# Optimization experiments

Hardware: AMD Instinct MI355X
Metric: run time of the kernel (lower is better)

Reference implementation:

```python
import jax, jax.numpy as jnp
import numpy as np
import math

B, S, E, H, L = 32, 512, 256, 8, 2
Dh = E // H
NUM_Q, NUM_C, MAX_POS, R = 10000, 200, 512, 4


def setup_inputs() -> dict:
    key = jax.random.key(0)
    ks = jax.random.split(key, 32)
    f = lambda k, sh: (jax.random.normal(k, sh, jnp.float32) * 0.05)
    que_emb = f(ks[0], (NUM_Q + 1, E)).at[0].set(0.0)  # padding_idx=0
    inp = dict(
        pid_data=jax.random.randint(ks[1], (B, S), 0, NUM_Q + 1),
        c_data=jax.random.randint(ks[2], (B, S, R), 0, NUM_C),
        target=jax.random.randint(ks[3], (B, S), 0, 2),
        que_emb=que_emb,
        concept_emb=f(ks[4], (NUM_C, E)),
        pos_key_emb=f(ks[5], (MAX_POS, Dh)),
        pos_value_emb=f(ks[6], (MAX_POS, Dh)),
        qc_W=f(ks[7], (2 * E, E)), qc_b=jnp.zeros((E,), jnp.float32),
        lin_W=f(ks[8], (2 * E, E)), lin_b=jnp.zeros((E,), jnp.float32),
        Wq=f(ks[9], (L, E, E)), bq=jnp.zeros((L, E), jnp.float32),
        Wk=f(ks[10], (L, E, E)), bk=jnp.zeros((L, E), jnp.float32),
        Wv=f(ks[11], (L, E, E)), bv=jnp.zeros((L, E), jnp.float32),
        o1_W=f(ks[12], (2 * E, E)), o1_b=jnp.zeros((E,), jnp.float32),
        o2_W=f(ks[13], (E, E)), o2_b=jnp.zeros((E,), jnp.float32),
        o3_W=f(ks[14], (E, 1)), o3_b=jnp.zeros((1,), jnp.float32),
    )
    return inp


def _relative_attention(q_in, v_in, Wq, bq, Wk, bk, Wv, bv, pos_key_emb, pos_value_emb):
    b, s, e = q_in.shape
    proj = lambda x, W, bias: (x @ W + bias).reshape(b, s, H, Dh).transpose(0, 2, 1, 3)
    q = proj(q_in, Wq, bq)  # [b,h,s,dh]
    k = proj(q_in, Wk, bk)
    v = proj(v_in, Wv, bv)
    # relative position indices, clamped (Shaw et al. variant)
    i = jnp.arange(s)
    idxs = jnp.clip(i[:, None] - i[None, :], 0, MAX_POS - 1)  # [s,s]
    pos_k = pos_key_emb[idxs]    # [s,s,dh]
    pos_v = pos_value_emb[idxs]  # [s,s,dh]
    scores = jnp.einsum('bhid,bhjd->bhij', q, k) + jnp.einsum('bhid,ijd->bhij', q, pos_k)
    scores = scores / math.sqrt(Dh)
    # future_mask: triu with k=0 -> mask j >= i (incl. diagonal)
    causal = (i[None, :] >= i[:, None])  # [s,s] True where masked
    scores = jnp.where(causal, jnp.float32(-1e9), scores)
    p = jax.nn.softmax(scores, axis=-1)  # [b,h,i,j]
    # pad-zero trick: row i=0 of attention replaced by zeros
    p = p * (i[:, None] > 0).astype(p.dtype)
    # value = v + per-pair positional value bias
    out = jnp.einsum('bhij,bhjd->bhid', p, v) + jnp.einsum('bhij,ijd->bhid', p, pos_v)
    return out.transpose(0, 2, 1, 3).reshape(b, s, E), p


def reference(pid_data, c_data, target, que_emb, concept_emb, pos_key_emb,
              pos_value_emb, qc_W, qc_b, lin_W, lin_b, Wq, bq, Wk, bk, Wv, bv,
              o1_W, o1_b, o2_W, o2_b, o3_W, o3_b):
    qemb = que_emb[pid_data]  # [B,S,E]
    # average skill embedding; index 0 of padded table is the zero/pad row
    concept_cat = jnp.concatenate([jnp.zeros((1, E), concept_emb.dtype), concept_emb], axis=0)
    related = c_data + 1  # [B,S,R]
    cemb_sum = concept_cat[related].sum(axis=-2)  # [B,S,E]
    cnt = (related != 0).sum(axis=-1, keepdims=True)
    cnt = jnp.maximum(cnt, 1)
    cemb = cemb_sum / cnt.astype(cemb_sum.dtype)
    query = jnp.concatenate([qemb, cemb], axis=-1) @ qc_W + qc_b  # [B,S,E]
    # interaction embedding gated by response label
    lbl = target[..., None].astype(query.dtype)
    inter = jnp.concatenate([query * lbl, query * (1.0 - lbl)], axis=-1)
    inter = jax.nn.relu(inter @ lin_W + lin_b)  # [B,S,E]
    sim = jax.nn.sigmoid(jnp.einsum('bse,ce->bsc', qemb, concept_emb))
    outputs, _ = _relative_attention(query, inter, Wq[0], bq[0], Wk[0], bk[0],
                                     Wv[0], bv[0], pos_key_emb, pos_value_emb)
    for l in range(1, L):
        residual, _ = _relative_attention(outputs, inter, Wq[l], bq[l], Wk[l], bk[l],
                                          Wv[l], bv[l], pos_key_emb, pos_value_emb)
        outputs = outputs + jax.nn.relu(residual)
    h = jnp.concatenate([outputs, query], axis=-1)
    h = jax.nn.relu(h @ o1_W + o1_b)
    h = jax.nn.relu(h @ o2_W + o2_b)
    pred = jax.nn.sigmoid((h @ o3_W + o3_b).squeeze(-1))  # [B,S]
    return pred, sim
```

## Files before the change

### kernel.cpp

```cpp
#include <hip/hip_runtime.h>
#include <hip/hip_bf16.h>
#include <cmath>

#define B_   32
#define S_   512
#define E_   256
#define H_   8
#define DH_  32
#define L_   2
#define R_   4
#define NUMC_ 200
#define MAXPOS_ 512
#define MTOK (B_ * S_)

typedef __attribute__((ext_vector_type(8))) short bf16x8_t;
typedef __attribute__((ext_vector_type(4))) float f32x4_t;

__device__ inline ushort bfu(float a) {
    union { __hip_bfloat16 h; ushort u; } x; x.h = __float2bfloat16(a); return x.u;
}
__device__ inline uint pk2bf(float a, float b) {
    return (uint)bfu(a) | ((uint)bfu(b) << 16);
}
__device__ inline float bf2f(ushort u) {
    union { float f; uint u; } x; x.u = (uint)u << 16; return x.f;
}
__device__ inline __hip_bfloat16 f2bf(float a) { return __float2bfloat16(a); }

__global__ __launch_bounds__(256) void wcvt_k(
    const float* __restrict__ qcW, const float* __restrict__ linW,
    const float* __restrict__ Wq, const float* __restrict__ Wk,
    const float* __restrict__ Wv, const float* __restrict__ o1W,
    const float* __restrict__ o2W, const float* __restrict__ ce,
    const float* __restrict__ posk, const float* __restrict__ posv,
    __hip_bfloat16* __restrict__ wb,
    __hip_bfloat16* __restrict__ pkPad, __hip_bfloat16* __restrict__ pvT)
{
    if (blockIdx.x >= 3584) {
        int t = (blockIdx.x - 3584) * 256 + threadIdx.x;
        {
            int row = t >> 5, d = t & 31;
            int rel = row - 32;
            float v = (rel >= 0 && rel < MAXPOS_) ? posk[(size_t)rel * DH_ + d] : 0.f;
            pkPad[t] = f2bf(v);
        }
        {
            int d = t / 576, c = t - d * 576;
            int rel = c - 31;
            float v = (rel >= 0 && rel < MAXPOS_) ? posv[(size_t)rel * DH_ + d] : 0.f;
            pvT[t] = f2bf(v);
        }
        return;
    }
    int i = blockIdx.x * 256 + threadIdx.x;
    float v;
    if (i < 131072) {
        int n = i >> 9, k = i & 511; v = qcW[k * 256 + n];
    } else if (i < 262144) {
        int l = i - 131072; int n = l >> 9, k = l & 511; v = linW[k * 256 + n];
    } else if (i < 524288) {
        int l2 = i - 262144; int ly = l2 >> 17; int r2 = l2 & 131071;
        int n = r2 >> 8, k = r2 & 255;
        v = (n < 256) ? Wq[ly * 65536 + k * 256 + n]
                      : Wk[ly * 65536 + k * 256 + (n - 256)];
    } else if (i < 655360) {
        int l2 = i - 524288; int n = l2 >> 8, k = l2 & 255;
        int ly = n >> 8, nn = n & 255;
        v = Wv[ly * 65536 + k * 256 + nn];
    } else if (i < 786432) {
        int l = i - 655360; int n = l >> 9, k = l & 511; v = o1W[k * 256 + n];
    } else if (i < 851968) {
        int l = i - 786432; int n = l >> 8, k = l & 255; v = o2W[k * 256 + n];
    } else {
        int l = i - 851968; int c = l >> 8, k = l & 255;
        v = (c < NUMC_) ? ce[c * 256 + k] : 0.f;
    }
    wb[i] = f2bf(v);
}

__global__ __launch_bounds__(256) void embed_k(
    const int* __restrict__ pid, const int* __restrict__ cdat,
    const float* __restrict__ qe, const float* __restrict__ ce,
    __hip_bfloat16* __restrict__ qemb, __hip_bfloat16* __restrict__ cemb)
{
    int tkn = blockIdx.x * 4 + (threadIdx.x >> 6);
    int e4  = (threadIdx.x & 63) * 4;
    int p = pid[tkn];
    float4 q = *reinterpret_cast<const float4*>(qe + (size_t)p * E_ + e4);
    ushort4 qo; qo.x = bfu(q.x); qo.y = bfu(q.y); qo.z = bfu(q.z); qo.w = bfu(q.w);
    *reinterpret_cast<ushort4*>(qemb + (size_t)tkn * E_ + e4) = qo;
    const int* c = cdat + (size_t)tkn * R_;
    float4 s = make_float4(0.f, 0.f, 0.f, 0.f);
#pragma unroll
    for (int r = 0; r < R_; ++r) {
        float4 v = *reinterpret_cast<const float4*>(ce + (size_t)c[r] * E_ + e4);
        s.x += v.x; s.y += v.y; s.z += v.z; s.w += v.w;
    }
    ushort4 co; co.x = bfu(s.x * 0.25f); co.y = bfu(s.y * 0.25f);
    co.z = bfu(s.z * 0.25f); co.w = bfu(s.w * 0.25f);
    *reinterpret_cast<ushort4*>(cemb + (size_t)tkn * E_ + e4) = co;
}

template<int AMODE, int EPI, int OMODE, int K, int NB>
__global__ __launch_bounds__(256) void gemm_bf_k(
    const __hip_bfloat16* __restrict__ A0, const __hip_bfloat16* __restrict__ A1,
    const int* __restrict__ lbl,
    const __hip_bfloat16* __restrict__ BT,
    const float* __restrict__ bias, const float* __restrict__ bias2,
    void* __restrict__ C0, void* __restrict__ C1, int Nstride)
{
    const int lane = threadIdx.x & 63, w = threadIdx.x >> 6;
    const int col = lane & 15, rg = lane >> 4;
    const int wr = w >> 1, wc = w & 1;
    int did = blockIdx.y * gridDim.x + blockIdx.x;
    int bm, bn;
    if (NB == 512) {
        int swz = (did & 7) * 128 + (did >> 3);
        bm = (swz >> 2) * 64; bn = (swz & 3) * 128;
    } else {
        int swz = (did & 7) * 64 + (did >> 3);
        bm = (swz >> 1) * 64; bn = (swz & 1) * 128;
    }
    const f32x4_t z4 = {0.f, 0.f, 0.f, 0.f};
    f32x4_t acc[2][4] = {{z4, z4, z4, z4}, {z4, z4, z4, z4}};
    const bf16x8_t z8 = {0, 0, 0, 0, 0, 0, 0, 0};

    int rowA[2];
    rowA[0] = bm + wr * 32 + col;
    rowA[1] = bm + wr * 32 + 16 + col;
    int lblv[2] = {0, 0};
    if (AMODE == 2) { lblv[0] = lbl[rowA[0]]; lblv[1] = lbl[rowA[1]]; }
    const int nb0 = bn + wc * 64;

    for (int k0 = 0; k0 < K; k0 += 32) {
        const int kk = k0 + 8 * rg;
        bf16x8_t af[2], bfr[4];
#pragma unroll
        for (int mt = 0; mt < 2; ++mt) {
            if (AMODE == 0) {
                af[mt] = *reinterpret_cast<const bf16x8_t*>(A0 + (size_t)rowA[mt] * K + kk);
            } else if (AMODE == 1) {
                const __hip_bfloat16* p = (kk < 256) ? (A0 + (size_t)rowA[mt] * 256 + kk)
                                                     : (A1 + (size_t)rowA[mt] * 256 + (kk - 256));
                af[mt] = *reinterpret_cast<const bf16x8_t*>(p);
            } else {
                bf16x8_t a = *reinterpret_cast<const bf16x8_t*>(A0 + (size_t)rowA[mt] * 256 + (kk & 255));
                bool first = (kk < 256);
                af[mt] = ((lblv[mt] != 0) == first) ? a : z8;
            }
        }
#pragma unroll
        for (int nt = 0; nt < 4; ++nt)
            bfr[nt] = *reinterpret_cast<const bf16x8_t*>(BT + (size_t)(nb0 + nt * 16 + col) * K + kk);

        __builtin_amdgcn_s_setprio(1);
#pragma unroll
        for (int mt = 0; mt < 2; ++mt)
#pragma unroll
        for (int nt = 0; nt < 4; ++nt)
            acc[mt][nt] = __builtin_amdgcn_mfma_f32_16x16x32_bf16(af[mt], bfr[nt], acc[mt][nt], 0, 0, 0);
        __builtin_amdgcn_s_setprio(0);
    }

#pragma unroll
    for (int mt = 0; mt < 2; ++mt)
#pragma unroll
    for (int nt = 0; nt < 4; ++nt) {
        const int n = nb0 + nt * 16 + col;
        const int mb = bm + wr * 32 + mt * 16 + 4 * rg;
        float bs = 0.f;
        if (bias) bs = (NB == 512 && n >= 256) ? bias2[n - 256] : bias[n];
        float xv[4];
#pragma unroll
        for (int r = 0; r < 4; ++r) {
            float x = acc[mt][nt][r] + bs;
            if (EPI == 1) x = fmaxf(x, 0.f);
            else if (EPI == 2) x = 1.f / (1.f + expf(-x));
            xv[r] = x;
        }
        if (OMODE == 0) {
            if (n < Nstride) {
                float* C = (float*)C0;
#pragma unroll
                for (int r = 0; r < 4; ++r)
                    C[(size_t)(mb + r) * Nstride + n] = xv[r];
            }
        } else if (OMODE == 3) {
            __hip_bfloat16* Cb = (__hip_bfloat16*)C0;
#pragma unroll
            for (int r = 0; r < 4; ++r)
                Cb[(size_t)(mb + r) * 256 + n] = f2bf(xv[r]);
        } else if (OMODE == 1) {
            __hip_bfloat16* dst = (n < 256) ? (__hip_bfloat16*)C0 : (__hip_bfloat16*)C1;
            const int nn = n & 255, hh = nn >> 5, d = nn & 31;
#pragma unroll
            for (int r = 0; r < 4; ++r) {
                int m = mb + r;
                int bh = (m >> 9) * 8 + hh;
                dst[((size_t)bh * 512 + (m & 511)) * 32 + d] = f2bf(xv[r]);
            }
        } else {
            __hip_bfloat16* dst = (n < 256) ? (__hip_bfloat16*)C0 : (__hip_bfloat16*)C1;
            const int nn = n & 255, hh = nn >> 5, d = nn & 31;
            const int bh = (mb >> 9) * 8 + hh;
            ushort4 pk;
            pk.x = bfu(xv[0]); pk.y = bfu(xv[1]); pk.z = bfu(xv[2]); pk.w = bfu(xv[3]);
            *reinterpret_cast<ushort4*>(dst + ((size_t)bh * 32 + d) * 512 + (mb & 511)) = pk;
        }
    }
}

__global__ __launch_bounds__(256) void gemm_pred_k(
    const __hip_bfloat16* __restrict__ A0, const __hip_bfloat16* __restrict__ BT,
    const float* __restrict__ b2, const float* __restrict__ w3,
    const float* __restrict__ b3, float* __restrict__ pred)
{
    __shared__ float sl[2][64];
    const int lane = threadIdx.x & 63, w = threadIdx.x >> 6;
    const int col = lane & 15, rg = lane >> 4;
    const int wr = w >> 1, wc = w & 1;
    const int bm = blockIdx.x * 64;

    const f32x4_t z4 = {0.f, 0.f, 0.f, 0.f};
    f32x4_t acc[2][8];
#pragma unroll
    for (int mt = 0; mt < 2; ++mt)
#pragma unroll
    for (int nt = 0; nt < 8; ++nt) acc[mt][nt] = z4;

    int rowA[2];
    rowA[0] = bm + wr * 32 + col;
    rowA[1] = bm + wr * 32 + 16 + col;
    const int nb0 = wc * 128;

    for (int k0 = 0; k0 < 256; k0 += 32) {
        const int kk = k0 + 8 * rg;
        bf16x8_t af[2], bfr[8];
#pragma unroll
        for (int mt = 0; mt < 2; ++mt)
            af[mt] = *reinterpret_cast<const bf16x8_t*>(A0 + (size_t)rowA[mt] * 256 + kk);
#pragma unroll
        for (int nt = 0; nt < 8; ++nt)
            bfr[nt] = *reinterpret_cast<const bf16x8_t*>(BT + (size_t)(nb0 + nt * 16 + col) * 256 + kk);
        __builtin_amdgcn_s_setprio(1);
#pragma unroll
        for (int mt = 0; mt < 2; ++mt)
#pragma unroll
        for (int nt = 0; nt < 8; ++nt)
            acc[mt][nt] = __builtin_amdgcn_mfma_f32_16x16x32_bf16(af[mt], bfr[nt], acc[mt][nt], 0, 0, 0);
        __builtin_amdgcn_s_setprio(0);
    }

    float pr[2][4] = {};
#pragma unroll
    for (int mt = 0; mt < 2; ++mt)
#pragma unroll
    for (int nt = 0; nt < 8; ++nt) {
        const int n = nb0 + nt * 16 + col;
        float bs = b2[n], wv = w3[n];
#pragma unroll
        for (int r = 0; r < 4; ++r)
            pr[mt][r] += fmaxf(acc[mt][nt][r] + bs, 0.f) * wv;
    }
#pragma unroll
    for (int mt = 0; mt < 2; ++mt)
#pragma unroll
    for (int r = 0; r < 4; ++r) {
        float v = pr[mt][r];
        v += __shfl_xor(v, 1); v += __shfl_xor(v, 2);
        v += __shfl_xor(v, 4); v += __shfl_xor(v, 8);
        if (col == 0) sl[wc][wr * 32 + mt * 16 + 4 * rg + r] = v;
    }
    __syncthreads();
    if (threadIdx.x < 64) {
        float s = sl[0][threadIdx.x] + sl[1][threadIdx.x] + b3[0];
        pred[bm + threadIdx.x] = 1.f / (1.f + expf(-s));
    }
}

#define QPST 36
template<int ADDREL>
__global__ __launch_bounds__(64) void attn1w_k(
    const __hip_bfloat16* __restrict__ Qbf, const __hip_bfloat16* __restrict__ Kbf,
    const __hip_bfloat16* __restrict__ Vt,  const __hip_bfloat16* __restrict__ pkPad,
    const __hip_bfloat16* __restrict__ pvT, __hip_bfloat16* __restrict__ outp)
{
    __shared__ __align__(16) ushort ldsA[64 * QPST];
    __shared__ __align__(16) ushort ldsP[2304];

    const int lane = threadIdx.x;
    const int col = lane & 15, rg = lane >> 4;
    const int bh = blockIdx.x, b = bh >> 3, h = bh & 7;
    const int band = 15 - blockIdx.y;
    const int i0 = band * 32;
    const int nT = band + 1;

    {
        uint4 zz = make_uint4(0u, 0u, 0u, 0u);
        uint4* pz = reinterpret_cast<uint4*>(ldsP);
#pragma unroll
        for (int t = 0; t < 5; ++t) {
            int idx = lane + 64 * t;
            if (idx < 288) pz[idx] = zz;
        }
    }

    const __hip_bfloat16* Qb = Qbf + (size_t)bh * 512 * 32;
    const __hip_bfloat16* Kb = Kbf + (size_t)bh * 512 * 32;
    const __hip_bfloat16* Vb = Vt  + (size_t)bh * 32 * 512;

    bf16x8_t qf[2];
    qf[0] = *reinterpret_cast<const bf16x8_t*>(Qb + (size_t)(i0 + col) * 32 + 8 * rg);
    qf[1] = *reinterpret_cast<const bf16x8_t*>(Qb + (size_t)(i0 + 16 + col) * 32 + 8 * rg);

    const f32x4_t z4 = {0.f, 0.f, 0.f, 0.f};
    f32x4_t o[2][2] = {{z4, z4}, {z4, z4}};
    float lrow[2][4] = {};
    const float rscale = 0.17677669529663687f;

    for (int t = 0; t < nT; ++t) {
        const int j0 = t * 32;
        bf16x8_t kf0 = *reinterpret_cast<const bf16x8_t*>(Kb + (size_t)(j0 + col) * 32 + 8 * rg);
        bf16x8_t kf1 = *reinterpret_cast<const bf16x8_t*>(Kb + (size_t)(j0 + 16 + col) * 32 + 8 * rg);
        const int prow0 = i0 - j0 + 1;
        bf16x8_t pkf[4];
#pragma unroll
        for (int rt = 0; rt < 4; ++rt)
            pkf[rt] = *reinterpret_cast<const bf16x8_t*>(
                pkPad + (size_t)(prow0 + rt * 16 + col) * 32 + 8 * rg);

        __builtin_amdgcn_s_setprio(1);
        f32x4_t sA[2][2];
        sA[0][0] = __builtin_amdgcn_mfma_f32_16x16x32_bf16(qf[0], kf0, z4, 0, 0, 0);
        sA[0][1] = __builtin_amdgcn_mfma_f32_16x16x32_bf16(qf[0], kf1, z4, 0, 0, 0);
        sA[1][0] = __builtin_amdgcn_mfma_f32_16x16x32_bf16(qf[1], kf0, z4, 0, 0, 0);
        sA[1][1] = __builtin_amdgcn_mfma_f32_16x16x32_bf16(qf[1], kf1, z4, 0, 0, 0);
        f32x4_t qp0[4], qp1[4];
#pragma unroll
        for (int rt = 0; rt < 4; ++rt) {
            qp0[rt] = __builtin_amdgcn_mfma_f32_16x16x32_bf16(qf[0], pkf[rt], z4, 0, 0, 0);
            qp1[rt] = __builtin_amdgcn_mfma_f32_16x16x32_bf16(qf[1], pkf[rt], z4, 0, 0, 0);
        }
        __builtin_amdgcn_s_setprio(0);

#pragma unroll
        for (int rt = 0; rt < 4; ++rt) {
            int xo = (rt * 16 + col) * QPST;
            uint2 wv;
            wv.x = pk2bf(qp0[rt][0], qp0[rt][1]);
            wv.y = pk2bf(qp0[rt][2], qp0[rt][3]);
            *reinterpret_cast<uint2*>(&ldsA[xo + 4 * rg]) = wv;
            wv.x = pk2bf(qp1[rt][0], qp1[rt][1]);
            wv.y = pk2bf(qp1[rt][2], qp1[rt][3]);
            *reinterpret_cast<uint2*>(&ldsA[xo + 16 + 4 * rg]) = wv;
        }

        const bool diag = (j0 == i0);
        float ev[2][2][4];
#pragma unroll
        for (int mt = 0; mt < 2; ++mt)
#pragma unroll
        for (int r = 0; r < 4; ++r) {
            const int ii = mt * 16 + 4 * rg + r;
#pragma unroll
            for (int nt = 0; nt < 2; ++nt) {
                const int jj = nt * 16 + col;
                float qpv = bf2f(ldsA[(ii - jj + 31) * QPST + ii]);
                float sc = (sA[mt][nt][r] + qpv) * rscale;
                float e = __expf(sc);
                if (diag && jj >= ii) e = 0.f;
                ev[mt][nt][r] = e;
            }
            lrow[mt][r] += ev[mt][0][r] + ev[mt][1][r];
        }

#pragma unroll
        for (int mt = 0; mt < 2; ++mt)
#pragma unroll
        for (int nt = 0; nt < 2; ++nt)
#pragma unroll
        for (int r = 0; r < 4; ++r) {
            const int ii = mt * 16 + 4 * rg + r;
            const int jj = nt * 16 + col;
            ushort pe = bfu(ev[mt][nt][r]);
            ldsA[ii * 32 + (jj ^ ((ii & 3) << 3))] = pe;
            ldsP[ii * 72 + (ii - jj + 31)] = pe;
        }

        bf16x8_t pa0 = *reinterpret_cast<const bf16x8_t*>(&ldsA[col * 32 + (8 * rg ^ ((col & 3) << 3))]);
        bf16x8_t pa1 = *reinterpret_cast<const bf16x8_t*>(&ldsA[(16 + col) * 32 + (8 * rg ^ ((col & 3) << 3))]);
        bf16x8_t vf0 = *reinterpret_cast<const bf16x8_t*>(Vb + (size_t)col * 512 + j0 + 8 * rg);
        bf16x8_t vf1 = *reinterpret_cast<const bf16x8_t*>(Vb + (size_t)(16 + col) * 512 + j0 + 8 * rg);
        bf16x8_t pr0[2], pr1[2], pv0[2], pv1[2];
#pragma unroll
        for (int ks = 0; ks < 2; ++ks) {
            pr0[ks] = *reinterpret_cast<const bf16x8_t*>(&ldsP[col * 72 + ks * 32 + 8 * rg]);
            pr1[ks] = *reinterpret_cast<const bf16x8_t*>(&ldsP[(16 + col) * 72 + ks * 32 + 8 * rg]);
            const __hip_bfloat16* pvb = pvT + (i0 - j0) + ks * 32 + 8 * rg;
            pv0[ks] = *reinterpret_cast<const bf16x8_t*>(pvb + (size_t)col * 576);
            pv1[ks] = *reinterpret_cast<const bf16x8_t*>(pvb + (size_t)(16 + col) * 576);
        }
        __builtin_amdgcn_s_setprio(1);
        o[0][0] = __builtin_amdgcn_mfma_f32_16x16x32_bf16(pa0, vf0, o[0][0], 0, 0, 0);
        o[0][1] = __builtin_amdgcn_mfma_f32_16x16x32_bf16(pa0, vf1, o[0][1], 0, 0, 0);
        o[1][0] = __builtin_amdgcn_mfma_f32_16x16x32_bf16(pa1, vf0, o[1][0], 0, 0, 0);
        o[1][1] = __builtin_amdgcn_mfma_f32_16x16x32_bf16(pa1, vf1, o[1][1], 0, 0, 0);
#pragma unroll
        for (int ks = 0; ks < 2; ++ks) {
            o[0][0] = __builtin_amdgcn_mfma_f32_16x16x32_bf16(pr0[ks], pv0[ks], o[0][0], 0, 0, 0);
            o[0][1] = __builtin_amdgcn_mfma_f32_16x16x32_bf16(pr0[ks], pv1[ks], o[0][1], 0, 0, 0);
            o[1][0] = __builtin_amdgcn_mfma_f32_16x16x32_bf16(pr1[ks], pv0[ks], o[1][0], 0, 0, 0);
            o[1][1] = __builtin_amdgcn_mfma_f32_16x16x32_bf16(pr1[ks], pv1[ks], o[1][1], 0, 0, 0);
        }
        __builtin_amdgcn_s_setprio(0);
    }

#pragma unroll
    for (int mt = 0; mt < 2; ++mt)
#pragma unroll
    for (int r = 0; r < 4; ++r) {
        float ls = lrow[mt][r];
        ls += __shfl_xor(ls, 1); ls += __shfl_xor(ls, 2);
        ls += __shfl_xor(ls, 4); ls += __shfl_xor(ls, 8);
        const int i = i0 + mt * 16 + 4 * rg + r;
        float inv = (i == 0) ? 0.f : 1.0f / ls;
        __hip_bfloat16* orow = outp + (size_t)(b * 512 + i) * 256 + h * 32;
        float v0 = o[mt][0][r] * inv;
        float v1 = o[mt][1][r] * inv;
        if (ADDREL) {
            v0 = bf2f(*(ushort*)&orow[col])      + fmaxf(v0, 0.f);
            v1 = bf2f(*(ushort*)&orow[16 + col]) + fmaxf(v1, 0.f);
        }
        orow[col]      = f2bf(v0);
        orow[16 + col] = f2bf(v1);
    }
}

extern "C" void kernel_launch(void* const* d_in, const int* in_sizes, int n_in,
                              void* d_out, int out_size, void* d_ws, size_t ws_size,
                              hipStream_t stream)
{
    const int*   pid        = (const int*)d_in[0];
    const int*   cdat       = (const int*)d_in[1];
    const int*   target     = (const int*)d_in[2];
    const float* que_emb    = (const float*)d_in[3];
    const float* concept_emb= (const float*)d_in[4];
    const float* posk       = (const float*)d_in[5];
    const float* posv       = (const float*)d_in[6];
    const float* qcW        = (const float*)d_in[7];
    const float* qcb        = (const float*)d_in[8];
    const float* linW       = (const float*)d_in[9];
    const float* linb       = (const float*)d_in[10];
    const float* Wq         = (const float*)d_in[11];
    const float* bq         = (const float*)d_in[12];
    const float* Wk         = (const float*)d_in[13];
    const float* bk         = (const float*)d_in[14];
    const float* Wv         = (const float*)d_in[15];
    const float* bv         = (const float*)d_in[16];
    const float* o1W        = (const float*)d_in[17];
    const float* o1b        = (const float*)d_in[18];
    const float* o2W        = (const float*)d_in[19];
    const float* o2b        = (const float*)d_in[20];
    const float* o3W        = (const float*)d_in[21];
    const float* o3b        = (const float*)d_in[22];

    float* out  = (float*)d_out;
    float* pred = out;
    float* sim  = out + MTOK;

    __hip_bfloat16* wsb = (__hip_bfloat16*)d_ws;
    const size_t HB = (size_t)MTOK * E_;
    __hip_bfloat16* qemb  = wsb + 0 * HB;
    __hip_bfloat16* cemb  = wsb + 1 * HB;
    __hip_bfloat16* query = wsb + 2 * HB;
    __hip_bfloat16* inter = wsb + 3 * HB;
    __hip_bfloat16* qbuf  = wsb + 4 * HB;
    __hip_bfloat16* kbuf  = wsb + 5 * HB;
    __hip_bfloat16* v0    = wsb + 6 * HB;
    __hip_bfloat16* v1    = wsb + 7 * HB;
    __hip_bfloat16* outp  = wsb + 8 * HB;
    __hip_bfloat16* h1    = wsb + 9 * HB;
    __hip_bfloat16* wb    = wsb + 10 * HB;
    __hip_bfloat16* qcWT  = wb;
    __hip_bfloat16* linWT = wb + 131072;
    __hip_bfloat16* wqkT  = wb + 262144;
    __hip_bfloat16* wvT   = wb + 524288;
    __hip_bfloat16* o1WT  = wb + 655360;
    __hip_bfloat16* o2WT  = wb + 786432;
    __hip_bfloat16* ceT   = wb + 851968;
    __hip_bfloat16* pkPad = wb + 917504;
    __hip_bfloat16* pvT   = pkPad + 18432;

    dim3 blk(256);
    dim3 g256(2, 256);
    dim3 g512(4, 256);
    dim3 gattn(B_ * H_, 16);
    dim3 blk64(64);

    wcvt_k<<<3656, blk, 0, stream>>>(qcW, linW, Wq, Wk, Wv, o1W, o2W, concept_emb,
                                     posk, posv, wb, pkPad, pvT);
    embed_k<<<MTOK / 4, blk, 0, stream>>>(pid, cdat, que_emb, concept_emb, qemb, cemb);

    gemm_bf_k<1, 0, 3, 512, 256><<<g256, blk, 0, stream>>>(qemb, cemb, nullptr, qcWT, qcb, nullptr, query, nullptr, 256);
    gemm_bf_k<2, 1, 3, 512, 256><<<g256, blk, 0, stream>>>(query, nullptr, target, linWT, linb, nullptr, inter, nullptr, 256);
    gemm_bf_k<0, 2, 0, 256, 256><<<g256, blk, 0, stream>>>(qemb, nullptr, nullptr, ceT, nullptr, nullptr, sim, nullptr, 200);
    gemm_bf_k<0, 0, 2, 256, 512><<<g512, blk, 0, stream>>>(inter, nullptr, nullptr, wvT, bv, bv + 256, v0, v1, 0);

    gemm_bf_k<0, 0, 1, 256, 512><<<g512, blk, 0, stream>>>(query, nullptr, nullptr, wqkT, bq, bk, qbuf, kbuf, 0);
    attn1w_k<0><<<gattn, blk64, 0, stream>>>(qbuf, kbuf, v0, pkPad, pvT, outp);

    gemm_bf_k<0, 0, 1, 256, 512><<<g512, blk, 0, stream>>>(outp, nullptr, nullptr, wqkT + 131072, bq + 256, bk + 256, qbuf, kbuf, 0);
    attn1w_k<1><<<gattn, blk64, 0, stream>>>(qbuf, kbuf, v1, pkPad, pvT, outp);

    gemm_bf_k<1, 1, 3, 512, 256><<<g256, blk, 0, stream>>>(outp, query, nullptr, o1WT, o1b, nullptr, h1, nullptr, 256);
    gemm_pred_k<<<256, blk, 0, stream>>>(h1, o2WT, o2b, o3W, o3b, pred);
}
```

Measured before the change: 290.7 us.

## Split attention query bands from 32 to 16 rows per wave

The single-wave attention kernel now handles 16 query rows per block instead of 32, doubling the grid in the band dimension. Per-block register and LDS footprint shrink (one Q fragment, three positional-key tiles, smaller scratch), and the causal mask moves to the last key tile. The aim is more parallelism and occupancy, with a shorter critical path for the longest bands. The cost is that K, V and positional tiles are loaded twice as often overall, and diagonal tiles do some masked work.

```diff
diff --git a/kernel.cpp b/kernel.cpp
--- a/kernel.cpp
+++ b/kernel.cpp
@@ -278,30 +278,30 @@
     }
 }
 
-#define QPST 36
+#define QPST 20
 template<int ADDREL>
 __global__ __launch_bounds__(64) void attn1w_k(
     const __hip_bfloat16* __restrict__ Qbf, const __hip_bfloat16* __restrict__ Kbf,
     const __hip_bfloat16* __restrict__ Vt,  const __hip_bfloat16* __restrict__ pkPad,
     const __hip_bfloat16* __restrict__ pvT, __hip_bfloat16* __restrict__ outp)
 {
-    __shared__ __align__(16) ushort ldsA[64 * QPST];
-    __shared__ __align__(16) ushort ldsP[2304];
+    __shared__ __align__(16) ushort ldsA[48 * QPST];
+    __shared__ __align__(16) ushort ldsP[16 * 72];
 
     const int lane = threadIdx.x;
     const int col = lane & 15, rg = lane >> 4;
     const int bh = blockIdx.x, b = bh >> 3, h = bh & 7;
-    const int band = 15 - blockIdx.y;
-    const int i0 = band * 32;
-    const int nT = band + 1;
+    const int band = 31 - (int)blockIdx.y;
+    const int i0 = band * 16;
+    const int nT = (band >> 1) + 1;
 
     {
         uint4 zz = make_uint4(0u, 0u, 0u, 0u);
         uint4* pz = reinterpret_cast<uint4*>(ldsP);
 #pragma unroll
-        for (int t = 0; t < 5; ++t) {
+        for (int t = 0; t < 3; ++t) {
             int idx = lane + 64 * t;
-            if (idx < 288) pz[idx] = zz;
+            if (idx < 144) pz[idx] = zz;
         }
     }
 
@@ -309,13 +309,11 @@
     const __hip_bfloat16* Kb = Kbf + (size_t)bh * 512 * 32;
     const __hip_bfloat16* Vb = Vt  + (size_t)bh * 32 * 512;
 
-    bf16x8_t qf[2];
-    qf[0] = *reinterpret_cast<const bf16x8_t*>(Qb + (size_t)(i0 + col) * 32 + 8 * rg);
-    qf[1] = *reinterpret_cast<const bf16x8_t*>(Qb + (size_t)(i0 + 16 + col) * 32 + 8 * rg);
+    bf16x8_t qf = *reinterpret_cast<const bf16x8_t*>(Qb + (size_t)(i0 + col) * 32 + 8 * rg);
 
     const f32x4_t z4 = {0.f, 0.f, 0.f, 0.f};
-    f32x4_t o[2][2] = {{z4, z4}, {z4, z4}};
-    float lrow[2][4] = {};
+    f32x4_t o[2] = {z4, z4};
+    float lrow[4] = {};
     const float rscale = 0.17677669529663687f;
 
     for (int t = 0; t < nT; ++t) {
@@ -323,110 +321,91 @@
         bf16x8_t kf0 = *reinterpret_cast<const bf16x8_t*>(Kb + (size_t)(j0 + col) * 32 + 8 * rg);
         bf16x8_t kf1 = *reinterpret_cast<const bf16x8_t*>(Kb + (size_t)(j0 + 16 + col) * 32 + 8 * rg);
         const int prow0 = i0 - j0 + 1;
-        bf16x8_t pkf[4];
-#pragma unroll
-        for (int rt = 0; rt < 4; ++rt)
+        bf16x8_t pkf[3];
+#pragma unroll
+        for (int rt = 0; rt < 3; ++rt)
             pkf[rt] = *reinterpret_cast<const bf16x8_t*>(
                 pkPad + (size_t)(prow0 + rt * 16 + col) * 32 + 8 * rg);
 
         __builtin_amdgcn_s_setprio(1);
-        f32x4_t sA[2][2];
-        sA[0][0] = __builtin_amdgcn_mfma_f32_16x16x32_bf16(qf[0], kf0, z4, 0, 0, 0);
-        sA[0][1] = __builtin_amdgcn_mfma_f32_16x16x32_bf16(qf[0], kf1, z4, 0, 0, 0);
-        sA[1][0] = __builtin_amdgcn_mfma_f32_16x16x32_bf16(qf[1], kf0, z4, 0, 0, 0);
-        sA[1][1] = __builtin_amdgcn_mfma_f32_16x16x32_bf16(qf[1], kf1, z4, 0, 0, 0);
-        f32x4_t qp0[4], qp1[4];
-#pragma unroll
-        for (int rt = 0; rt < 4; ++rt) {
-            qp0[rt] = __builtin_amdgcn_mfma_f32_16x16x32_bf16(qf[0], pkf[rt], z4, 0, 0, 0);
-            qp1[rt] = __builtin_amdgcn_mfma_f32_16x16x32_bf16(qf[1], pkf[rt], z4, 0, 0, 0);
-        }
+        f32x4_t sA[2];
+        sA[0] = __builtin_amdgcn_mfma_f32_16x16x32_bf16(qf, kf0, z4, 0, 0, 0);
+        sA[1] = __builtin_amdgcn_mfma_f32_16x16x32_bf16(qf, kf1, z4, 0, 0, 0);
+        f32x4_t qp[3];
+#pragma unroll
+        for (int rt = 0; rt < 3; ++rt)
+            qp[rt] = __builtin_amdgcn_mfma_f32_16x16x32_bf16(qf, pkf[rt], z4, 0, 0, 0);
         __builtin_amdgcn_s_setprio(0);
 
 #pragma unroll
-        for (int rt = 0; rt < 4; ++rt) {
+        for (int rt = 0; rt < 3; ++rt) {
             int xo = (rt * 16 + col) * QPST;
             uint2 wv;
-            wv.x = pk2bf(qp0[rt][0], qp0[rt][1]);
-            wv.y = pk2bf(qp0[rt][2], qp0[rt][3]);
+            wv.x = pk2bf(qp[rt][0], qp[rt][1]);
+            wv.y = pk2bf(qp[rt][2], qp[rt][3]);
             *reinterpret_cast<uint2*>(&ldsA[xo + 4 * rg]) = wv;
-            wv.x = pk2bf(qp1[rt][0], qp1[rt][1]);
-            wv.y = pk2bf(qp1[rt][2], qp1[rt][3]);
-            *reinterpret_cast<uint2*>(&ldsA[xo + 16 + 4 * rg]) = wv;
-        }
-
-        const bool diag = (j0 == i0);
-        float ev[2][2][4];
-#pragma unroll
-        for (int mt = 0; mt < 2; ++mt)
+        }
+
+        const bool last = (t == nT - 1);
+        float ev[2][4];
 #pragma unroll
         for (int r = 0; r < 4; ++r) {
-            const int ii = mt * 16 + 4 * rg + r;
+            const int ii = 4 * rg + r;
 #pragma unroll
             for (int nt = 0; nt < 2; ++nt) {
                 const int jj = nt * 16 + col;
                 float qpv = bf2f(ldsA[(ii - jj + 31) * QPST + ii]);
-                float sc = (sA[mt][nt][r] + qpv) * rscale;
+                float sc = (sA[nt][r] + qpv) * rscale;
                 float e = __expf(sc);
-                if (diag && jj >= ii) e = 0.f;
-                ev[mt][nt][r] = e;
+                if (last && (j0 + jj >= i0 + ii)) e = 0.f;
+                ev[nt][r] = e;
             }
-            lrow[mt][r] += ev[mt][0][r] + ev[mt][1][r];
-        }
-
-#pragma unroll
-        for (int mt = 0; mt < 2; ++mt)
+            lrow[r] += ev[0][r] + ev[1][r];
+        }
+
 #pragma unroll
         for (int nt = 0; nt < 2; ++nt)
 #pragma unroll
         for (int r = 0; r < 4; ++r) {
-            const int ii = mt * 16 + 4 * rg + r;
+            const int ii = 4 * rg + r;
             const int jj = nt * 16 + col;
-            ushort pe = bfu(ev[mt][nt][r]);
+            ushort pe = bfu(ev[nt][r]);
             ldsA[ii * 32 + (jj ^ ((ii & 3) << 3))] = pe;
             ldsP[ii * 72 + (ii - jj + 31)] = pe;
         }
 
-        bf16x8_t pa0 = *reinterpret_cast<const bf16x8_t*>(&ldsA[col * 32 + (8 * rg ^ ((col & 3) << 3))]);
-        bf16x8_t pa1 = *reinterpret_cast<const bf16x8_t*>(&ldsA[(16 + col) * 32 + (8 * rg ^ ((col & 3) << 3))]);
+        bf16x8_t pa = *reinterpret_cast<const bf16x8_t*>(&ldsA[col * 32 + (8 * rg ^ ((col & 3) << 3))]);
         bf16x8_t vf0 = *reinterpret_cast<const bf16x8_t*>(Vb + (size_t)col * 512 + j0 + 8 * rg);
         bf16x8_t vf1 = *reinterpret_cast<const bf16x8_t*>(Vb + (size_t)(16 + col) * 512 + j0 + 8 * rg);
-        bf16x8_t pr0[2], pr1[2], pv0[2], pv1[2];
+        bf16x8_t pr[2], pv0[2], pv1[2];
 #pragma unroll
         for (int ks = 0; ks < 2; ++ks) {
-            pr0[ks] = *reinterpret_cast<const bf16x8_t*>(&ldsP[col * 72 + ks * 32 + 8 * rg]);
-            pr1[ks] = *reinterpret_cast<const bf16x8_t*>(&ldsP[(16 + col) * 72 + ks * 32 + 8 * rg]);
+            pr[ks] = *reinterpret_cast<const bf16x8_t*>(&ldsP[col * 72 + ks * 32 + 8 * rg]);
             const __hip_bfloat16* pvb = pvT + (i0 - j0) + ks * 32 + 8 * rg;
             pv0[ks] = *reinterpret_cast<const bf16x8_t*>(pvb + (size_t)col * 576);
             pv1[ks] = *reinterpret_cast<const bf16x8_t*>(pvb + (size_t)(16 + col) * 576);
         }
         __builtin_amdgcn_s_setprio(1);
-        o[0][0] = __builtin_amdgcn_mfma_f32_16x16x32_bf16(pa0, vf0, o[0][0], 0, 0, 0);
-        o[0][1] = __builtin_amdgcn_mfma_f32_16x16x32_bf16(pa0, vf1, o[0][1], 0, 0, 0);
-        o[1][0] = __builtin_amdgcn_mfma_f32_16x16x32_bf16(pa1, vf0, o[1][0], 0, 0, 0);
-        o[1][1] = __builtin_amdgcn_mfma_f32_16x16x32_bf16(pa1, vf1, o[1][1], 0, 0, 0);
+        o[0] = __builtin_amdgcn_mfma_f32_16x16x32_bf16(pa, vf0, o[0], 0, 0, 0);
+        o[1] = __builtin_amdgcn_mfma_f32_16x16x32_bf16(pa, vf1, o[1], 0, 0, 0);
 #pragma unroll
         for (int ks = 0; ks < 2; ++ks) {
-            o[0][0] = __builtin_amdgcn_mfma_f32_16x16x32_bf16(pr0[ks], pv0[ks], o[0][0], 0, 0, 0);
-            o[0][1] = __builtin_amdgcn_mfma_f32_16x16x32_bf16(pr0[ks], pv1[ks], o[0][1], 0, 0, 0);
-            o[1][0] = __builtin_amdgcn_mfma_f32_16x16x32_bf16(pr1[ks], pv0[ks], o[1][0], 0, 0, 0);
-            o[1][1] = __builtin_amdgcn_mfma_f32_16x16x32_bf16(pr1[ks], pv1[ks], o[1][1], 0, 0, 0);
+            o[0] = __builtin_amdgcn_mfma_f32_16x16x32_bf16(pr[ks], pv0[ks], o[0], 0, 0, 0);
+            o[1] = __builtin_amdgcn_mfma_f32_16x16x32_bf16(pr[ks], pv1[ks], o[1], 0, 0, 0);
         }
         __builtin_amdgcn_s_setprio(0);
     }
 
 #pragma unroll
-    for (int mt = 0; mt < 2; ++mt)
-#pragma unroll
     for (int r = 0; r < 4; ++r) {
-        float ls = lrow[mt][r];
+        float ls = lrow[r];
         ls += __shfl_xor(ls, 1); ls += __shfl_xor(ls, 2);
         ls += __shfl_xor(ls, 4); ls += __shfl_xor(ls, 8);
-        const int i = i0 + mt * 16 + 4 * rg + r;
+        const int i = i0 + 4 * rg + r;
         float inv = (i == 0) ? 0.f : 1.0f / ls;
         __hip_bfloat16* orow = outp + (size_t)(b * 512 + i) * 256 + h * 32;
-        float v0 = o[mt][0][r] * inv;
-        float v1 = o[mt][1][r] * inv;
+        float v0 = o[0][r] * inv;
+        float v1 = o[1][r] * inv;
         if (ADDREL) {
             v0 = bf2f(*(ushort*)&orow[col])      + fmaxf(v0, 0.f);
             v1 = bf2f(*(ushort*)&orow[16 + col]) + fmaxf(v1, 0.f);
@@ -494,7 +473,7 @@
     dim3 blk(256);
     dim3 g256(2, 256);
     dim3 g512(4, 256);
-    dim3 gattn(B_ * H_, 16);
+    dim3 gattn(B_ * H_, 32);
     dim3 blk64(64);
 
     wcvt_k<<<3656, blk, 0, stream>>>(qcW, linW, Wq, Wk, Wv, o1W, o2W, concept_emb,
```

New measurement: 350.0 us. +20.4%, slower.

## Fuse sim GEMM into query projection and fuse head MLP GEMMs

Applied to the files above, without the earlier changes.

Concatenates the padded concept embedding into the query-projection weight so one GEMM produces both query and sigmoid similarity. Fuses the o1 and o2 GEMMs and prediction head into one kernel keeping the hidden activations in LDS, removing the h1 buffer round-trip and two launches. Also vectorizes the weight conversion kernel to 8 elements per thread. The merged GEMM does redundant MFMA work on zero-padded K for the sim columns.

```diff
diff --git a/kernel.cpp b/kernel.cpp
--- a/kernel.cpp
+++ b/kernel.cpp
@@ -36,8 +36,8 @@
     __hip_bfloat16* __restrict__ wb,
     __hip_bfloat16* __restrict__ pkPad, __hip_bfloat16* __restrict__ pvT)
 {
-    if (blockIdx.x >= 3584) {
-        int t = (blockIdx.x - 3584) * 256 + threadIdx.x;
+    if (blockIdx.x >= 480) {
+        int t = (blockIdx.x - 480) * 256 + threadIdx.x;
         {
             int row = t >> 5, d = t & 31;
             int rel = row - 32;
@@ -52,30 +52,53 @@
         }
         return;
     }
-    int i = blockIdx.x * 256 + threadIdx.x;
-    float v;
-    if (i < 131072) {
-        int n = i >> 9, k = i & 511; v = qcW[k * 256 + n];
-    } else if (i < 262144) {
-        int l = i - 131072; int n = l >> 9, k = l & 511; v = linW[k * 256 + n];
-    } else if (i < 524288) {
-        int l2 = i - 262144; int ly = l2 >> 17; int r2 = l2 & 131071;
-        int n = r2 >> 8, k = r2 & 255;
-        v = (n < 256) ? Wq[ly * 65536 + k * 256 + n]
-                      : Wk[ly * 65536 + k * 256 + (n - 256)];
-    } else if (i < 655360) {
-        int l2 = i - 524288; int n = l2 >> 8, k = l2 & 255;
-        int ly = n >> 8, nn = n & 255;
-        v = Wv[ly * 65536 + k * 256 + nn];
-    } else if (i < 786432) {
-        int l = i - 655360; int n = l >> 9, k = l & 511; v = o1W[k * 256 + n];
-    } else if (i < 851968) {
-        int l = i - 786432; int n = l >> 8, k = l & 255; v = o2W[k * 256 + n];
+    int id8 = blockIdx.x * 256 + threadIdx.x;
+    float v[8];
+    size_t dst;
+    if (id8 < 16384) {
+        int n = id8 & 255, k0 = (id8 >> 8) * 8;
+#pragma unroll
+        for (int j = 0; j < 8; ++j) v[j] = qcW[(size_t)(k0 + j) * 256 + n];
+        dst = (size_t)n * 512 + k0;
+    } else if (id8 < 32768) {
+        int l = id8 - 16384; int c = l & 255, k0 = (l >> 8) * 8;
+#pragma unroll
+        for (int j = 0; j < 8; ++j)
+            v[j] = (c < NUMC_ && k0 < 256) ? ce[(size_t)c * 256 + k0 + j] : 0.f;
+        dst = 131072 + (size_t)c * 512 + k0;
+    } else if (id8 < 49152) {
+        int l = id8 - 32768; int n = l & 255, k0 = (l >> 8) * 8;
+#pragma unroll
+        for (int j = 0; j < 8; ++j) v[j] = linW[(size_t)(k0 + j) * 256 + n];
+        dst = 262144 + (size_t)n * 512 + k0;
+    } else if (id8 < 81920) {
+        int l = id8 - 49152; int n2 = l & 1023, k0 = (l >> 10) * 8;
+        int ly = n2 >> 9, n = n2 & 511;
+        const float* src = (n < 256) ? (Wq + ly * 65536 + n) : (Wk + ly * 65536 + (n - 256));
+#pragma unroll
+        for (int j = 0; j < 8; ++j) v[j] = src[(size_t)(k0 + j) * 256];
+        dst = 393216 + (size_t)n2 * 256 + k0;
+    } else if (id8 < 98304) {
+        int l = id8 - 81920; int n = l & 511, k0 = (l >> 9) * 8;
+        const float* src = Wv + (n >> 8) * 65536 + (n & 255);
+#pragma unroll
+        for (int j = 0; j < 8; ++j) v[j] = src[(size_t)(k0 + j) * 256];
+        dst = 655360 + (size_t)n * 256 + k0;
+    } else if (id8 < 114688) {
+        int l = id8 - 98304; int n = l & 255, k0 = (l >> 8) * 8;
+#pragma unroll
+        for (int j = 0; j < 8; ++j) v[j] = o1W[(size_t)(k0 + j) * 256 + n];
+        dst = 786432 + (size_t)n * 512 + k0;
     } else {
-        int l = i - 851968; int c = l >> 8, k = l & 255;
-        v = (c < NUMC_) ? ce[c * 256 + k] : 0.f;
-    }
-    wb[i] = f2bf(v);
+        int l = id8 - 114688; int n = l & 255, k0 = (l >> 8) * 8;
+#pragma unroll
+        for (int j = 0; j < 8; ++j) v[j] = o2W[(size_t)(k0 + j) * 256 + n];
+        dst = 917504 + (size_t)n * 256 + k0;
+    }
+    union { ushort u[8]; uint4 q; } pk;
+#pragma unroll
+    for (int j = 0; j < 8; ++j) pk.u[j] = bfu(v[j]);
+    *reinterpret_cast<uint4*>(wb + dst) = pk.q;
 }
 
 __global__ __launch_bounds__(256) void embed_k(
@@ -169,13 +192,15 @@
         const int n = nb0 + nt * 16 + col;
         const int mb = bm + wr * 32 + mt * 16 + 4 * rg;
         float bs = 0.f;
-        if (bias) bs = (NB == 512 && n >= 256) ? bias2[n - 256] : bias[n];
+        if (OMODE == 4) bs = (n < 256 && bias) ? bias[n] : 0.f;
+        else if (bias) bs = (NB == 512 && n >= 256) ? bias2[n - 256] : bias[n];
         float xv[4];
 #pragma unroll
         for (int r = 0; r < 4; ++r) {
             float x = acc[mt][nt][r] + bs;
             if (EPI == 1) x = fmaxf(x, 0.f);
             else if (EPI == 2) x = 1.f / (1.f + expf(-x));
+            if (OMODE == 4 && n >= 256) x = 1.f / (1.f + expf(-x));
             xv[r] = x;
         }
         if (OMODE == 0) {
@@ -190,6 +215,18 @@
 #pragma unroll
             for (int r = 0; r < 4; ++r)
                 Cb[(size_t)(mb + r) * 256 + n] = f2bf(xv[r]);
+        } else if (OMODE == 4) {
+            if (n < 256) {
+                __hip_bfloat16* Cb = (__hip_bfloat16*)C0;
+#pragma unroll
+                for (int r = 0; r < 4; ++r)
+                    Cb[(size_t)(mb + r) * 256 + n] = f2bf(xv[r]);
+            } else if (n - 256 < NUMC_) {
+                float* S = (float*)C1;
+#pragma unroll
+                for (int r = 0; r < 4; ++r)
+                    S[(size_t)(mb + r) * NUMC_ + (n - 256)] = xv[r];
+            }
         } else if (OMODE == 1) {
             __hip_bfloat16* dst = (n < 256) ? (__hip_bfloat16*)C0 : (__hip_bfloat16*)C1;
             const int nn = n & 255, hh = nn >> 5, d = nn & 31;
@@ -210,66 +247,114 @@
     }
 }
 
-__global__ __launch_bounds__(256) void gemm_pred_k(
-    const __hip_bfloat16* __restrict__ A0, const __hip_bfloat16* __restrict__ BT,
-    const float* __restrict__ b2, const float* __restrict__ w3,
-    const float* __restrict__ b3, float* __restrict__ pred)
+#define HST 264
+__global__ __launch_bounds__(256) void head_k(
+    const __hip_bfloat16* __restrict__ A0, const __hip_bfloat16* __restrict__ A1,
+    const __hip_bfloat16* __restrict__ o1WT, const float* __restrict__ b1,
+    const __hip_bfloat16* __restrict__ o2WT, const float* __restrict__ b2,
+    const float* __restrict__ w3, const float* __restrict__ b3,
+    float* __restrict__ pred)
 {
+    __shared__ __align__(16) ushort ldsH[64 * HST];
     __shared__ float sl[2][64];
     const int lane = threadIdx.x & 63, w = threadIdx.x >> 6;
     const int col = lane & 15, rg = lane >> 4;
     const int wr = w >> 1, wc = w & 1;
     const int bm = blockIdx.x * 64;
-
+    const int nb0 = wc * 128;
     const f32x4_t z4 = {0.f, 0.f, 0.f, 0.f};
-    f32x4_t acc[2][8];
-#pragma unroll
-    for (int mt = 0; mt < 2; ++mt)
-#pragma unroll
-    for (int nt = 0; nt < 8; ++nt) acc[mt][nt] = z4;
 
     int rowA[2];
     rowA[0] = bm + wr * 32 + col;
     rowA[1] = bm + wr * 32 + 16 + col;
-    const int nb0 = wc * 128;
-
-    for (int k0 = 0; k0 < 256; k0 += 32) {
-        const int kk = k0 + 8 * rg;
-        bf16x8_t af[2], bfr[8];
-#pragma unroll
-        for (int mt = 0; mt < 2; ++mt)
-            af[mt] = *reinterpret_cast<const bf16x8_t*>(A0 + (size_t)rowA[mt] * 256 + kk);
-#pragma unroll
-        for (int nt = 0; nt < 8; ++nt)
-            bfr[nt] = *reinterpret_cast<const bf16x8_t*>(BT + (size_t)(nb0 + nt * 16 + col) * 256 + kk);
-        __builtin_amdgcn_s_setprio(1);
-#pragma unroll
-        for (int mt = 0; mt < 2; ++mt)
-#pragma unroll
-        for (int nt = 0; nt < 8; ++nt)
-            acc[mt][nt] = __builtin_amdgcn_mfma_f32_16x16x32_bf16(af[mt], bfr[nt], acc[mt][nt], 0, 0, 0);
-        __builtin_amdgcn_s_setprio(0);
-    }
-
-    float pr[2][4] = {};
-#pragma unroll
-    for (int mt = 0; mt < 2; ++mt)
-#pragma unroll
-    for (int nt = 0; nt < 8; ++nt) {
-        const int n = nb0 + nt * 16 + col;
-        float bs = b2[n], wv = w3[n];
-#pragma unroll
-        for (int r = 0; r < 4; ++r)
-            pr[mt][r] += fmaxf(acc[mt][nt][r] + bs, 0.f) * wv;
-    }
-#pragma unroll
-    for (int mt = 0; mt < 2; ++mt)
-#pragma unroll
-    for (int r = 0; r < 4; ++r) {
-        float v = pr[mt][r];
-        v += __shfl_xor(v, 1); v += __shfl_xor(v, 2);
-        v += __shfl_xor(v, 4); v += __shfl_xor(v, 8);
-        if (col == 0) sl[wc][wr * 32 + mt * 16 + 4 * rg + r] = v;
+
+    {
+        f32x4_t acc[2][8];
+#pragma unroll
+        for (int mt = 0; mt < 2; ++mt)
+#pragma unroll
+        for (int nt = 0; nt < 8; ++nt) acc[mt][nt] = z4;
+
+        for (int k0 = 0; k0 < 512; k0 += 32) {
+            const int kk = k0 + 8 * rg;
+            bf16x8_t af[2], bfr[8];
+#pragma unroll
+            for (int mt = 0; mt < 2; ++mt) {
+                const __hip_bfloat16* p = (kk < 256) ? (A0 + (size_t)rowA[mt] * 256 + kk)
+                                                     : (A1 + (size_t)rowA[mt] * 256 + (kk - 256));
+                af[mt] = *reinterpret_cast<const bf16x8_t*>(p);
+            }
+#pragma unroll
+            for (int nt = 0; nt < 8; ++nt)
+                bfr[nt] = *reinterpret_cast<const bf16x8_t*>(o1WT + (size_t)(nb0 + nt * 16 + col) * 512 + kk);
+            __builtin_amdgcn_s_setprio(1);
+#pragma unroll
+            for (int mt = 0; mt < 2; ++mt)
+#pragma unroll
+            for (int nt = 0; nt < 8; ++nt)
+                acc[mt][nt] = __builtin_amdgcn_mfma_f32_16x16x32_bf16(af[mt], bfr[nt], acc[mt][nt], 0, 0, 0);
+            __builtin_amdgcn_s_setprio(0);
+        }
+#pragma unroll
+        for (int mt = 0; mt < 2; ++mt)
+#pragma unroll
+        for (int nt = 0; nt < 8; ++nt) {
+            const int n = nb0 + nt * 16 + col;
+            const float bs = b1[n];
+            const int rb = wr * 32 + mt * 16 + 4 * rg;
+#pragma unroll
+            for (int r = 0; r < 4; ++r)
+                ldsH[(rb + r) * HST + n] = bfu(fmaxf(acc[mt][nt][r] + bs, 0.f));
+        }
+    }
+    __syncthreads();
+
+    {
+        f32x4_t acc[2][8];
+#pragma unroll
+        for (int mt = 0; mt < 2; ++mt)
+#pragma unroll
+        for (int nt = 0; nt < 8; ++nt) acc[mt][nt] = z4;
+
+        for (int k0 = 0; k0 < 256; k0 += 32) {
+            const int kk = k0 + 8 * rg;
+            bf16x8_t af[2], bfr[8];
+#pragma unroll
+            for (int mt = 0; mt < 2; ++mt)
+                af[mt] = *reinterpret_cast<const bf16x8_t*>(
+                    &ldsH[(wr * 32 + mt * 16 + col) * HST + kk]);
+#pragma unroll
+            for (int nt = 0; nt < 8; ++nt)
+                bfr[nt] = *reinterpret_cast<const bf16x8_t*>(o2WT + (size_t)(nb0 + nt * 16 + col) * 256 + kk);
+            __builtin_amdgcn_s_setprio(1);
+#pragma unroll
+            for (int mt = 0; mt < 2; ++mt)
+#pragma unroll
+            for (int nt = 0; nt < 8; ++nt)
+                acc[mt][nt] = __builtin_amdgcn_mfma_f32_16x16x32_bf16(af[mt], bfr[nt], acc[mt][nt], 0, 0, 0);
+            __builtin_amdgcn_s_setprio(0);
+        }
+
+        float pr[2][4] = {};
+#pragma unroll
+        for (int mt = 0; mt < 2; ++mt)
+#pragma unroll
+        for (int nt = 0; nt < 8; ++nt) {
+            const int n = nb0 + nt * 16 + col;
+            float bs = b2[n], wv = w3[n];
+#pragma unroll
+            for (int r = 0; r < 4; ++r)
+                pr[mt][r] += fmaxf(acc[mt][nt][r] + bs, 0.f) * wv;
+        }
+#pragma unroll
+        for (int mt = 0; mt < 2; ++mt)
+#pragma unroll
+        for (int r = 0; r < 4; ++r) {
+            float v = pr[mt][r];
+            v += __shfl_xor(v, 1); v += __shfl_xor(v, 2);
+            v += __shfl_xor(v, 4); v += __shfl_xor(v, 8);
+            if (col == 0) sl[wc][wr * 32 + mt * 16 + 4 * rg + r] = v;
+        }
     }
     __syncthreads();
     if (threadIdx.x < 64) {
@@ -479,16 +564,14 @@
     __hip_bfloat16* v0    = wsb + 6 * HB;
     __hip_bfloat16* v1    = wsb + 7 * HB;
     __hip_bfloat16* outp  = wsb + 8 * HB;
-    __hip_bfloat16* h1    = wsb + 9 * HB;
-    __hip_bfloat16* wb    = wsb + 10 * HB;
-    __hip_bfloat16* qcWT  = wb;
-    __hip_bfloat16* linWT = wb + 131072;
-    __hip_bfloat16* wqkT  = wb + 262144;
-    __hip_bfloat16* wvT   = wb + 524288;
-    __hip_bfloat16* o1WT  = wb + 655360;
-    __hip_bfloat16* o2WT  = wb + 786432;
-    __hip_bfloat16* ceT   = wb + 851968;
-    __hip_bfloat16* pkPad = wb + 917504;
+    __hip_bfloat16* wb    = wsb + 9 * HB;
+    __hip_bfloat16* qcCe  = wb;
+    __hip_bfloat16* linWT = wb + 262144;
+    __hip_bfloat16* wqkT  = wb + 393216;
+    __hip_bfloat16* wvT   = wb + 655360;
+    __hip_bfloat16* o1WT  = wb + 786432;
+    __hip_bfloat16* o2WT  = wb + 917504;
+    __hip_bfloat16* pkPad = wb + 983040;
     __hip_bfloat16* pvT   = pkPad + 18432;
 
     dim3 blk(256);
@@ -497,13 +580,12 @@
     dim3 gattn(B_ * H_, 16);
     dim3 blk64(64);
 
-    wcvt_k<<<3656, blk, 0, stream>>>(qcW, linW, Wq, Wk, Wv, o1W, o2W, concept_emb,
-                                     posk, posv, wb, pkPad, pvT);
+    wcvt_k<<<552, blk, 0, stream>>>(qcW, linW, Wq, Wk, Wv, o1W, o2W, concept_emb,
+                                    posk, posv, wb, pkPad, pvT);
     embed_k<<<MTOK / 4, blk, 0, stream>>>(pid, cdat, que_emb, concept_emb, qemb, cemb);
 
-    gemm_bf_k<1, 0, 3, 512, 256><<<g256, blk, 0, stream>>>(qemb, cemb, nullptr, qcWT, qcb, nullptr, query, nullptr, 256);
+    gemm_bf_k<1, 0, 4, 512, 512><<<g512, blk, 0, stream>>>(qemb, cemb, nullptr, qcCe, qcb, nullptr, query, sim, 0);
     gemm_bf_k<2, 1, 3, 512, 256><<<g256, blk, 0, stream>>>(query, nullptr, target, linWT, linb, nullptr, inter, nullptr, 256);
-    gemm_bf_k<0, 2, 0, 256, 256><<<g256, blk, 0, stream>>>(qemb, nullptr, nullptr, ceT, nullptr, nullptr, sim, nullptr, 200);
     gemm_bf_k<0, 0, 2, 256, 512><<<g512, blk, 0, stream>>>(inter, nullptr, nullptr, wvT, bv, bv + 256, v0, v1, 0);
 
     gemm_bf_k<0, 0, 1, 256, 512><<<g512, blk, 0, stream>>>(query, nullptr, nullptr, wqkT, bq, bk, qbuf, kbuf, 0);
@@ -512,6 +594,5 @@
     gemm_bf_k<0, 0, 1, 256, 512><<<g512, blk, 0, stream>>>(outp, nullptr, nullptr, wqkT + 131072, bq + 256, bk + 256, qbuf, kbuf, 0);
     attn1w_k<1><<<gattn, blk64, 0, stream>>>(qbuf, kbuf, v1, pkPad, pvT, outp);
 
-    gemm_bf_k<1, 1, 3, 512, 256><<<g256, blk, 0, stream>>>(outp, query, nullptr, o1WT, o1b, nullptr, h1, nullptr, 256);
-    gemm_pred_k<<<256, blk, 0, stream>>>(h1, o2WT, o2b, o3W, o3b, pred);
-}
+    head_k<<<256, blk, 0, stream>>>(outp, query, o1WT, o1b, o2WT, o2b, o3W, o3b, pred);
+}
```

New measurement: 288.1 us. About the same (-0.9%).
